# Kernel tuning notes

Measured on AMD Instinct MI355X. Metric: run time of the kernel, lower is better.

The kernel has to match this reference:

```python
import jax, jax.numpy as jnp
import numpy as np

BLOCK_SIZE = 32
TAU = 0.1
E2M1_VALUES = np.array([0.0, 0.5, 1.0, 1.5, 2.0, 3.0, 4.0, 6.0], dtype=np.float32)
E2M1_BOUNDS = np.array([0.25, 0.75, 1.25, 1.75, 2.5, 3.5, 5.0], dtype=np.float32)


def setup_inputs() -> dict:
    key = jax.random.key(0)
    x = jax.random.normal(key, (2048, 4096), dtype=jnp.float32)
    return {
        "x": x,
        "delta_raw": jnp.zeros((), dtype=jnp.float32),
        "bounds_base": jnp.asarray(E2M1_BOUNDS),
        "values_table": jnp.asarray(E2M1_VALUES),
    }


def reference(x, delta_raw, bounds_base, values_table):
    orig_shape = x.shape
    bs = BLOCK_SIZE
    xb = x.reshape(-1, bs)  # [n_blocks, bs]
    # per-block e8m0 power-of-two scale from amax
    amax = jnp.max(jnp.abs(xb), axis=-1, keepdims=True)
    descale = amax / 6.0
    e8m0_scale = jnp.ceil(jnp.maximum(jnp.log2(descale), -127.0))
    scale_factor = jnp.exp2(e8m0_scale)
    x_scaled = (xb / scale_factor).reshape(orig_shape)
    # perturbed decision bounds
    shifted_bounds = bounds_base + 0.5 * jnp.tanh(delta_raw)  # [7]
    x_abs = jnp.abs(x_scaled)
    # hard ordinal bucketize: count bounds exceeded -> code in [0,7]
    ord_hard = jnp.sum(x_abs[..., None] > shifted_bounds, axis=-1)  # int32
    sign_bit = (x_scaled < 0).astype(jnp.uint8)
    codes = (sign_bit << 3) | ord_hard.astype(jnp.uint8)
    # soft ordinal weights via sigmoid at each boundary
    p = jax.nn.sigmoid((x_abs[..., None] - shifted_bounds) / TAU)  # [..., 7]
    w0 = 1.0 - p[..., 0]
    mids = p[..., :-1] - p[..., 1:]
    w_last = p[..., -1]
    weights = jnp.concatenate([w0[..., None], mids, w_last[..., None]], axis=-1)  # [..., 8]
    weights = jnp.clip(weights, 0.0)
    weights = weights / (jnp.sum(weights, axis=-1, keepdims=True) + 1e-8)
    abs_soft = jnp.sum(weights * values_table, axis=-1)
    abs_hard = values_table[ord_hard]
    # straight-through: hard value forward, soft gradient
    abs_mix = abs_soft + jax.lax.stop_gradient(abs_hard - abs_soft)
    y_scaled = jnp.where(x_scaled >= 0, abs_mix, -abs_mix)
    y = (y_scaled.reshape(-1, bs) * scale_factor).reshape(orig_shape)
    scales = (e8m0_scale + 127.0).astype(jnp.uint8)[:, 0].reshape(
        *orig_shape[:-1], orig_shape[-1] // bs
    )
    return (y, codes, scales, shifted_bounds, weights)
```

## Files before the change

### kernel.cpp

```cpp
#include <hip/hip_runtime.h>

#define BLK 256

__global__ __launch_bounds__(BLK) void fp4_kernel(
    const float* __restrict__ x,
    const float* __restrict__ delta_raw,
    const float* __restrict__ bounds_base,
    const float* __restrict__ values_table,
    float* __restrict__ out, long long N)
{
    const int tid = threadIdx.x;
    const long long gid = (long long)blockIdx.x * BLK + tid;

    __shared__ float s_vals[8];
    __shared__ float s_w[8 * 264];

    if (tid < 8) s_vals[tid] = values_table[tid];

    const float delta = delta_raw[0];
    const float ht = 0.5f * tanhf(delta);
    float sb[7];
#pragma unroll
    for (int j = 0; j < 7; ++j) sb[j] = bounds_base[j] + ht;

    __syncthreads();

    const float xi = x[gid];

    float a = fabsf(xi);
#pragma unroll
    for (int off = 16; off >= 1; off >>= 1)
        a = fmaxf(a, __shfl_xor(a, off, 32));

    const float descale = a / 6.0f;
    const float e = ceilf(fmaxf(log2f(descale), -127.0f));
    const float scale = exp2f(e);
    const float xs = xi / scale;
    const float xa = fabsf(xs);

    int ord = 0;
    float p[7];
#pragma unroll
    for (int j = 0; j < 7; ++j) {
        if (xa > sb[j]) ord++;
        p[j] = 1.0f / (1.0f + expf(-((xa - sb[j]) / 0.1f)));
    }

    float w[8];
    w[0] = 1.0f - p[0];
#pragma unroll
    for (int j = 1; j < 7; ++j) w[j] = p[j - 1] - p[j];
    w[7] = p[6];

    float sum = 0.0f;
#pragma unroll
    for (int k = 0; k < 8; ++k) { w[k] = fmaxf(w[k], 0.0f); sum += w[k]; }
    const float inv = 1.0f / (sum + 1e-8f);

    float abs_soft = 0.0f;
#pragma unroll
    for (int k = 0; k < 8; ++k) { w[k] *= inv; abs_soft += w[k] * s_vals[k]; }

    const float abs_hard = s_vals[ord];
    const float abs_mix = abs_soft + (abs_hard - abs_soft);
    const float ys = (xs >= 0.0f) ? abs_mix : -abs_mix;

    out[gid] = ys * scale;
    const int code = ((xs < 0.0f) ? 8 : 0) | ord;
    out[N + gid] = (float)code;
    if ((tid & 31) == 0) out[2 * N + (gid >> 5)] = e + 127.0f;
    if (blockIdx.x == 0 && tid < 7) out[2 * N + (N >> 5) + tid] = sb[tid];

#pragma unroll
    for (int j = 0; j < 8; ++j) s_w[j * 264 + tid] = w[j];
    __syncthreads();

    const long long wbase = 2 * N + (N >> 5) + 7 + (long long)blockIdx.x * (BLK * 8);
#pragma unroll
    for (int k = 0; k < 8; ++k) {
        const int g = tid + k * BLK;
        out[wbase + g] = s_w[(g & 7) * 264 + (g >> 3)];
    }
}

extern "C" void kernel_launch(void* const* d_in, const int* in_sizes, int n_in,
                              void* d_out, int out_size, void* d_ws, size_t ws_size,
                              hipStream_t stream) {
    const float* x      = (const float*)d_in[0];
    const float* delta  = (const float*)d_in[1];
    const float* bounds = (const float*)d_in[2];
    const float* vals   = (const float*)d_in[3];
    float* out = (float*)d_out;
    const long long N = (long long)in_sizes[0];
    const int nblocks = (int)(N / BLK);
    fp4_kernel<<<nblocks, BLK, 0, stream>>>(x, delta, bounds, vals, out, N);
}
```

Before: 393.7 us.

## Process four elements per thread with vectorized IO and swizzled LDS weight staging

Each thread now handles four contiguous elements, loading and storing them with float4 and cutting the block amax reduction to three shuffles. Sigmoids use exp2 with prescaled bounds and hardware reciprocal, and the power-of-two scale is built by bit manipulation instead of a divide. The per-element weights are staged in a larger XOR-swizzled LDS buffer and written out coalesced. The trade-off is a 32 KB LDS footprint per block, which may lower occupancy, plus approximate reciprocals that can shift low-order bits of the weights.

```diff
diff --git a/kernel.cpp b/kernel.cpp
--- a/kernel.cpp
+++ b/kernel.cpp
@@ -1,6 +1,8 @@
 #include <hip/hip_runtime.h>
 
 #define BLK 256
+#define EPT 4
+#define WLDS (BLK * EPT * 8)
 
 __global__ __launch_bounds__(BLK) void fp4_kernel(
     const float* __restrict__ x,
@@ -10,76 +12,100 @@
     float* __restrict__ out, long long N)
 {
     const int tid = threadIdx.x;
-    const long long gid = (long long)blockIdx.x * BLK + tid;
+    const long long base = (long long)blockIdx.x * (BLK * EPT);
+    const long long g0 = base + (long long)(tid * EPT);
 
     __shared__ float s_vals[8];
-    __shared__ float s_w[8 * 264];
+    __shared__ __align__(16) float s_w[WLDS];
 
     if (tid < 8) s_vals[tid] = values_table[tid];
 
-    const float delta = delta_raw[0];
-    const float ht = 0.5f * tanhf(delta);
-    float sb[7];
+    const float ht = 0.5f * tanhf(delta_raw[0]);
+    const float C = 14.426950408889634f;
+    float sb[7], cb[7];
 #pragma unroll
-    for (int j = 0; j < 7; ++j) sb[j] = bounds_base[j] + ht;
+    for (int j = 0; j < 7; ++j) { sb[j] = bounds_base[j] + ht; cb[j] = sb[j] * C; }
+    float vt[8];
+#pragma unroll
+    for (int k = 0; k < 8; ++k) vt[k] = values_table[k];
 
     __syncthreads();
 
-    const float xi = x[gid];
+    const float4 xv = *reinterpret_cast<const float4*>(x + g0);
+    const float xe[EPT] = {xv.x, xv.y, xv.z, xv.w};
 
-    float a = fabsf(xi);
-#pragma unroll
-    for (int off = 16; off >= 1; off >>= 1)
-        a = fmaxf(a, __shfl_xor(a, off, 32));
+    float a = fmaxf(fmaxf(fabsf(xe[0]), fabsf(xe[1])),
+                    fmaxf(fabsf(xe[2]), fabsf(xe[3])));
+    a = fmaxf(a, __shfl_xor(a, 1));
+    a = fmaxf(a, __shfl_xor(a, 2));
+    a = fmaxf(a, __shfl_xor(a, 4));
 
     const float descale = a / 6.0f;
     const float e = ceilf(fmaxf(log2f(descale), -127.0f));
-    const float scale = exp2f(e);
-    const float xs = xi / scale;
-    const float xa = fabsf(xs);
+    const int ie = (int)e;
+    const float inv_scale = __int_as_float((127 - ie) << 23);
+    const float scale = (ie == -127) ? __int_as_float(0x00400000)
+                                     : __int_as_float((ie + 127) << 23);
 
-    int ord = 0;
-    float p[7];
+    const int wkey = (tid & 7) << 2;
+    float ys[EPT], cd[EPT];
+
 #pragma unroll
-    for (int j = 0; j < 7; ++j) {
-        if (xa > sb[j]) ord++;
-        p[j] = 1.0f / (1.0f + expf(-((xa - sb[j]) / 0.1f)));
+    for (int i = 0; i < EPT; ++i) {
+        const float xs = xe[i] * inv_scale;
+        const float xa = fabsf(xs);
+
+        int ord = 0;
+#pragma unroll
+        for (int j = 0; j < 7; ++j) ord += (xa > sb[j]) ? 1 : 0;
+
+        const float xac = xa * C;
+        float p[7];
+#pragma unroll
+        for (int j = 0; j < 7; ++j) {
+            const float ex = exp2f(cb[j] - xac);
+            p[j] = __builtin_amdgcn_rcpf(1.0f + ex);
+        }
+
+        float w[8];
+        w[0] = 1.0f - p[0];
+#pragma unroll
+        for (int j = 1; j < 7; ++j) w[j] = p[j - 1] - p[j];
+        w[7] = p[6];
+
+        float sum = 0.0f;
+#pragma unroll
+        for (int k = 0; k < 8; ++k) { w[k] = fmaxf(w[k], 0.0f); sum += w[k]; }
+        const float inv = __builtin_amdgcn_rcpf(sum + 1e-8f);
+
+        float abs_soft = 0.0f;
+#pragma unroll
+        for (int k = 0; k < 8; ++k) { w[k] *= inv; abs_soft += w[k] * vt[k]; }
+
+        const float abs_hard = s_vals[ord];
+        const float abs_mix = abs_soft + (abs_hard - abs_soft);
+        ys[i] = ((xs >= 0.0f) ? abs_mix : -abs_mix) * scale;
+        cd[i] = (float)(((xs < 0.0f) ? 8 : 0) | ord);
+
+        const int f = (tid * EPT + i) * 8;
+        *reinterpret_cast<float4*>(&s_w[(f + 0) ^ wkey]) =
+            make_float4(w[0], w[1], w[2], w[3]);
+        *reinterpret_cast<float4*>(&s_w[(f + 4) ^ wkey]) =
+            make_float4(w[4], w[5], w[6], w[7]);
     }
 
-    float w[8];
-    w[0] = 1.0f - p[0];
-#pragma unroll
-    for (int j = 1; j < 7; ++j) w[j] = p[j - 1] - p[j];
-    w[7] = p[6];
-
-    float sum = 0.0f;
-#pragma unroll
-    for (int k = 0; k < 8; ++k) { w[k] = fmaxf(w[k], 0.0f); sum += w[k]; }
-    const float inv = 1.0f / (sum + 1e-8f);
-
-    float abs_soft = 0.0f;
-#pragma unroll
-    for (int k = 0; k < 8; ++k) { w[k] *= inv; abs_soft += w[k] * s_vals[k]; }
-
-    const float abs_hard = s_vals[ord];
-    const float abs_mix = abs_soft + (abs_hard - abs_soft);
-    const float ys = (xs >= 0.0f) ? abs_mix : -abs_mix;
-
-    out[gid] = ys * scale;
-    const int code = ((xs < 0.0f) ? 8 : 0) | ord;
-    out[N + gid] = (float)code;
-    if ((tid & 31) == 0) out[2 * N + (gid >> 5)] = e + 127.0f;
+    *reinterpret_cast<float4*>(out + g0)     = make_float4(ys[0], ys[1], ys[2], ys[3]);
+    *reinterpret_cast<float4*>(out + N + g0) = make_float4(cd[0], cd[1], cd[2], cd[3]);
+    if ((tid & 7) == 0) out[2 * N + (g0 >> 5)] = e + 127.0f;
     if (blockIdx.x == 0 && tid < 7) out[2 * N + (N >> 5) + tid] = sb[tid];
 
-#pragma unroll
-    for (int j = 0; j < 8; ++j) s_w[j * 264 + tid] = w[j];
     __syncthreads();
 
-    const long long wbase = 2 * N + (N >> 5) + 7 + (long long)blockIdx.x * (BLK * 8);
+    const long long wbase = 2 * N + (N >> 5) + 7 + (long long)blockIdx.x * WLDS;
+    const int rbase = tid ^ (((tid >> 5) & 7) << 2);
 #pragma unroll
-    for (int k = 0; k < 8; ++k) {
-        const int g = tid + k * BLK;
-        out[wbase + g] = s_w[(g & 7) * 264 + (g >> 3)];
+    for (int k = 0; k < 32; ++k) {
+        out[wbase + tid + (k << 8)] = s_w[rbase + (k << 8)];
     }
 }
 
@@ -92,6 +118,6 @@
     const float* vals   = (const float*)d_in[3];
     float* out = (float*)d_out;
     const long long N = (long long)in_sizes[0];
-    const int nblocks = (int)(N / BLK);
+    const int nblocks = (int)(N / (BLK * EPT));
     fp4_kernel<<<nblocks, BLK, 0, stream>>>(x, delta, bounds, vals, out, N);
 }
```

Result: faster. 358.3 us (-9.0%).
